# Optimization experiments

Hardware: AMD Instinct MI355X
Metric: run time of the kernel (lower is better)

Reference implementation:

```python
import jax, jax.numpy as jnp
import numpy as np

NUM_HEADS = 16
HEAD_DIM = 64  # hidden_dim // num_heads = 1024 // 16

def setup_inputs() -> dict:
    key = jax.random.key(0)
    ks = jax.random.split(key, 6)
    B, T, H, W, D = 2, 16, 24, 24, 1024
    s = 0.02
    return {
        "x": jax.random.normal(ks[0], (B, T * H * W, D), jnp.float32),
        "ws_qkv": jax.random.normal(ks[1], (D, 3 * D), jnp.float32) * s,
        "bs_qkv": jnp.zeros((3 * D,), jnp.float32),
        "ws_proj": jax.random.normal(ks[2], (D, D), jnp.float32) * s,
        "bs_proj": jnp.zeros((D,), jnp.float32),
        "wt_qkv": jax.random.normal(ks[3], (D, 3 * D), jnp.float32) * s,
        "bt_qkv": jnp.zeros((3 * D,), jnp.float32),
        "wt_proj": jax.random.normal(ks[4], (D, D), jnp.float32) * s,
        "bt_proj": jnp.zeros((D,), jnp.float32),
        "T": 16, "H": 24, "W": 24,
    }

def _heads(x):
    # [..., N, D] -> [..., nh, N, hd]
    *lead, N, D = x.shape
    x = x.reshape(*lead, N, NUM_HEADS, HEAD_DIM)
    return jnp.swapaxes(x, -2, -3)

def _attend(q, k, v, causal):
    # q,k,v: [..., nh, N, hd]
    scores = jnp.einsum("...qd,...kd->...qk", q, k) / jnp.sqrt(jnp.float32(HEAD_DIM))
    if causal:
        N = q.shape[-2]
        mask = jnp.triu(jnp.ones((N, N), bool), k=1)
        scores = jnp.where(mask, jnp.float32(-jnp.inf), scores)
    attn = jax.nn.softmax(scores, axis=-1)
    out = jnp.einsum("...qk,...kd->...qd", attn, v)
    # [..., nh, N, hd] -> [..., N, D]
    out = jnp.swapaxes(out, -2, -3)
    return out.reshape(*out.shape[:-2], NUM_HEADS * HEAD_DIM)

def _spatial(x, w_qkv, b_qkv, w_proj, b_proj, T, HW):
    B, THW, D = x.shape
    qkv = x @ w_qkv + b_qkv
    q, k, v = jnp.split(qkv, 3, axis=-1)
    # group tokens by frame: [B, T, HW, D]
    q, k, v = (t.reshape(B, T, HW, D) for t in (q, k, v))
    out = _attend(_heads(q), _heads(k), _heads(v), causal=False)
    out = out.reshape(B, THW, D)
    return out @ w_proj + b_proj

def _temporal(x, w_qkv, b_qkv, w_proj, b_proj, T, HW, causal):
    B, THW, D = x.shape
    qkv = x @ w_qkv + b_qkv
    q, k, v = jnp.split(qkv, 3, axis=-1)
    # group tokens by spatial position: [B, HW, T, D]
    q, k, v = (jnp.swapaxes(t.reshape(B, T, HW, D), 1, 2) for t in (q, k, v))
    out = _attend(_heads(q), _heads(k), _heads(v), causal=causal)  # [B, HW, T, D]
    out = jnp.swapaxes(out, 1, 2).reshape(B, THW, D)
    return out @ w_proj + b_proj

def reference(x, ws_qkv, bs_qkv, ws_proj, bs_proj, wt_qkv, bt_qkv, wt_proj, bt_proj, T, H, W):
    HW = H * W
    x = x + _spatial(x, ws_qkv, bs_qkv, ws_proj, bs_proj, T, HW)
    x = x + _temporal(x, wt_qkv, bt_qkv, wt_proj, bt_proj, T, HW, causal=True)
    return x
```

## Files before the change

kernel.cpp:

```cpp
#include <hip/hip_runtime.h>
#include <math.h>

typedef __bf16 bf16_t;
typedef unsigned char u8;
typedef __bf16 bf16x4 __attribute__((ext_vector_type(4)));
typedef __bf16 bf16x8 __attribute__((ext_vector_type(8)));
typedef float f32x4 __attribute__((ext_vector_type(4)));

#define GLDS(gp, lp) __builtin_amdgcn_global_load_lds( \
    (const __attribute__((address_space(1))) void*)(gp), \
    (__attribute__((address_space(3))) void*)(lp), 16, 0, 0)

static constexpr int B_    = 2;
static constexpr int T_    = 16;
static constexpr int HW_   = 576;
static constexpr int NH_   = 16;
static constexpr int TOK_  = B_ * T_ * HW_;
static constexpr int D_    = 1024;
static constexpr int D3_   = 3072;

#define GEMM_PROLOG_AND_KLOOP(AS, BS)                                         \
    const int tid  = threadIdx.x;                                             \
    const int lane = tid & 63, wid = tid >> 6;                                \
    const int wr   = wid >> 1, wc = wid & 1;                                  \
    const int l15  = lane & 15, lhi = lane >> 4;                              \
    const int cpx = gridDim.x >> 3;                                           \
    const int swz = (blockIdx.x & 7) * cpx + (blockIdx.x >> 3);               \
    const long row0 = (long)(swz / ntx) * 128;                                \
    const long col0 = (long)(swz % ntx) * 128;                                \
    const int  sr   = tid >> 2;                                               \
    const int  sc   = (((tid & 3) ^ ((sr >> 1) & 3)) * 8);                    \
    const bf16_t* Ag = A  + (row0 + sr) * (long)K + sc;                       \
    const bf16_t* Bg = BT + (col0 + sr) * (long)K + sc;                       \
    f32x4 acc[4][4] = {};                                                     \
    GLDS(Ag,                AS(0) + tid * 8);                                 \
    GLDS(Ag + 64 * (long)K, AS(0) + 2048 + tid * 8);                          \
    GLDS(Bg,                BS(0) + tid * 8);                                 \
    GLDS(Bg + 64 * (long)K, BS(0) + 2048 + tid * 8);                          \
    __syncthreads();                                                          \
    const int nt = K >> 5;                                                    \
    int cur = 0;                                                              \
    for (int t = 0; t < nt; ++t) {                                            \
        if (t + 1 < nt) {                                                     \
            const int k0 = (t + 1) << 5;                                      \
            GLDS(Ag + k0,                AS(cur ^ 1) + tid * 8);              \
            GLDS(Ag + 64 * (long)K + k0, AS(cur ^ 1) + 2048 + tid * 8);       \
            GLDS(Bg + k0,                BS(cur ^ 1) + tid * 8);              \
            GLDS(Bg + 64 * (long)K + k0, BS(cur ^ 1) + 2048 + tid * 8);       \
        }                                                                     \
        bf16x8 a[4], b[4];                                                    \
        _Pragma("unroll")                                                     \
        for (int i = 0; i < 4; i++) {                                         \
            const int Ra = wr * 64 + i * 16 + l15;                            \
            a[i] = *(const bf16x8*)(AS(cur) + Ra * 32                         \
                                    + ((lhi ^ ((Ra >> 1) & 3)) * 8));         \
        }                                                                     \
        _Pragma("unroll")                                                     \
        for (int j = 0; j < 4; j++) {                                         \
            const int Rb = wc * 64 + j * 16 + l15;                            \
            b[j] = *(const bf16x8*)(BS(cur) + Rb * 32                         \
                                    + ((lhi ^ ((Rb >> 1) & 3)) * 8));         \
        }                                                                     \
        __builtin_amdgcn_s_setprio(1);                                        \
        _Pragma("unroll")                                                     \
        for (int i = 0; i < 4; i++)                                           \
            _Pragma("unroll")                                                 \
            for (int j = 0; j < 4; j++)                                       \
                acc[i][j] = __builtin_amdgcn_mfma_f32_16x16x32_bf16(a[i], b[j], acc[i][j], 0, 0, 0); \
        __builtin_amdgcn_s_setprio(0);                                        \
        __syncthreads();                                                      \
        cur ^= 1;                                                             \
    }

__global__ __launch_bounds__(256) void prep(const float* __restrict__ x,
                                            u8* __restrict__ x_f8,
                                            const float* __restrict__ wqs,
                                            u8* __restrict__ wTqs8,
                                            const float* __restrict__ wps,
                                            bf16_t* __restrict__ wTps,
                                            const float* __restrict__ wqt,
                                            u8* __restrict__ wTqt8,
                                            const float* __restrict__ wpt,
                                            bf16_t* __restrict__ wTpt)
{
    const int bid = blockIdx.x, tid = threadIdx.x;
    if (bid < 4096) {
        const long n = (long)TOK_ * D_;
        for (long i = ((long)bid * 256 + tid) * 8; i < n; i += 4096L * 256 * 8) {
            const float4 v0 = *(const float4*)(x + i);
            const float4 v1 = *(const float4*)(x + i + 4);
            int lo = __builtin_amdgcn_cvt_pk_fp8_f32(v0.x, v0.y, 0, false);
            lo = __builtin_amdgcn_cvt_pk_fp8_f32(v0.z, v0.w, lo, true);
            int hi = __builtin_amdgcn_cvt_pk_fp8_f32(v1.x, v1.y, 0, false);
            hi = __builtin_amdgcn_cvt_pk_fp8_f32(v1.z, v1.w, hi, true);
            int2 p; p.x = lo; p.y = hi;
            *(int2*)(x_f8 + i) = p;
        }
        return;
    }
    const float* in; u8* out8 = nullptr; bf16_t* outb = nullptr; int C, b2;
    if (bid < 7168)       { in = wqs; out8 = wTqs8; C = 3072; b2 = bid - 4096; }
    else if (bid < 8192)  { in = wps; outb = wTps;  C = 1024; b2 = bid - 7168; }
    else if (bid < 11264) { in = wqt; out8 = wTqt8; C = 3072; b2 = bid - 8192; }
    else                  { in = wpt; outb = wTpt;  C = 1024; b2 = bid - 11264; }
    const int nbx = C >> 5;
    const int cb = (b2 % nbx) * 32, rb = (b2 / nbx) * 32;
    const int tx = tid & 31, ty = tid >> 5;
    __shared__ float tile[32][33];
    #pragma unroll
    for (int i = 0; i < 32; i += 8)
        tile[ty + i][tx] = in[(long)(rb + ty + i) * C + cb + tx];
    __syncthreads();
    if (out8) {
        #pragma unroll
        for (int i = 0; i < 32; i += 8) {
            const int p = __builtin_amdgcn_cvt_pk_fp8_f32(tile[tx][ty + i], 0.f, 0, false);
            out8[(long)(cb + ty + i) * 1024 + rb + tx] = (u8)(p & 0xff);
        }
    } else {
        #pragma unroll
        for (int i = 0; i < 32; i += 8)
            outb[(long)(cb + ty + i) * 1024 + rb + tx] = (bf16_t)tile[tx][ty + i];
    }
}

__global__ __launch_bounds__(256) void b2f8(const bf16_t* __restrict__ in,
                                            u8* __restrict__ out, long n)
{
    for (long i = ((long)blockIdx.x * 256 + threadIdx.x) * 8; i < n;
         i += (long)gridDim.x * 256 * 8) {
        bf16x8 v = *(const bf16x8*)(in + i);
        int lo = __builtin_amdgcn_cvt_pk_fp8_f32((float)v[0], (float)v[1], 0, false);
        lo = __builtin_amdgcn_cvt_pk_fp8_f32((float)v[2], (float)v[3], lo, true);
        int hi = __builtin_amdgcn_cvt_pk_fp8_f32((float)v[4], (float)v[5], 0, false);
        hi = __builtin_amdgcn_cvt_pk_fp8_f32((float)v[6], (float)v[7], hi, true);
        int2 p; p.x = lo; p.y = hi;
        *(int2*)(out + i) = p;
    }
}

__global__ __launch_bounds__(256) void gemm_f8(const u8* __restrict__ A,
                                               const u8* __restrict__ BT,
                                               const float* __restrict__ bias,
                                               bf16_t* __restrict__ Cb,
                                               bf16_t* __restrict__ vout,
                                               int vmode, int ntx,
                                               int M, int N, int K, int tperm)
{
    __shared__ bf16_t SHm[16384];
    char* SH = (char*)SHm;
    const int tid  = threadIdx.x;
    const int lane = tid & 63, wid = tid >> 6;
    const int wr   = wid >> 1, wc = wid & 1;
    const int l15  = lane & 15, lhi = lane >> 4;
    const int cpx = gridDim.x >> 3;
    const int swz = (blockIdx.x & 7) * cpx + (blockIdx.x >> 3);
    const long row0 = (long)(swz / ntx) * 128;
    const long col0 = (long)(swz % ntx) * 128;
    const int crow = tid >> 2, cq = tid & 3;

#define STG8(Xp, rbase, kt, dst) do {                                         \
        _Pragma("unroll")                                                     \
        for (int i_ = 0; i_ < 2; i_++) {                                      \
            const int row_ = crow + i_ * 64;                                  \
            GLDS(Xp + (rbase + row_) * (long)K + (kt) * 64                    \
                 + ((cq ^ ((row_ >> 1) & 3)) * 16),                           \
                 (dst) + (row_ * 64 + cq * 16));                              \
        }                                                                     \
    } while (0)

    f32x4 acc[4][4] = {};

    STG8(A,  row0, 0, SH);
    STG8(BT, col0, 0, SH + 16384);
    __syncthreads();

    const int NT = K >> 6;
    int cur = 0;
    for (int t = 0; t < NT; ++t) {
        if (t + 1 < NT) {
            STG8(A,  row0, t + 1, SH + (cur ^ 1) * 8192);
            STG8(BT, col0, t + 1, SH + 16384 + (cur ^ 1) * 8192);
        }

        long av[4][2], bv[4][2];
        #pragma unroll
        for (int i = 0; i < 4; i++) {
            const int Ra = wr * 64 + i * 16 + l15;
            const int x2 = ((Ra >> 1) & 3) << 1;
            #pragma unroll
            for (int kk = 0; kk < 2; kk++)
                av[i][kk] = *(const long*)(SH + cur * 8192 + Ra * 64
                                           + (((kk * 4 + lhi) ^ x2) * 8));
        }
        #pragma unroll
        for (int j = 0; j < 4; j++) {
            const int Rb = wc * 64 + j * 16 + l15;
            const int x2 = ((Rb >> 1) & 3) << 1;
            #pragma unroll
            for (int kk = 0; kk < 2; kk++)
                bv[j][kk] = *(const long*)(SH + 16384 + cur * 8192 + Rb * 64
                                           + (((kk * 4 + lhi) ^ x2) * 8));
        }

        __builtin_amdgcn_s_setprio(1);
        #pragma unroll
        for (int i = 0; i < 4; i++)
            #pragma unroll
            for (int j = 0; j < 4; j++) {
                acc[i][j] = __builtin_amdgcn_mfma_f32_16x16x32_fp8_fp8(av[i][0], bv[j][0], acc[i][j], 0, 0, 0);
                acc[i][j] = __builtin_amdgcn_mfma_f32_16x16x32_fp8_fp8(av[i][1], bv[j][1], acc[i][j], 0, 0, 0);
            }
        __builtin_amdgcn_s_setprio(0);
        __syncthreads();
        cur ^= 1;
    }
#undef STG8

    if (!(vmode == 1 && col0 >= 2048)) {
        #pragma unroll
        for (int i = 0; i < 4; i++) {
            #pragma unroll
            for (int j = 0; j < 4; j++) {
                const long col  = col0 + wc * 64 + j * 16 + l15;
                const int  lrow0 = wr * 64 + i * 16 + lhi * 4;
                const int  lcol  = wc * 64 + j * 16 + l15;
                #pragma unroll
                for (int r = 0; r < 4; r++)
                    SHm[(lrow0 + r) * 128 + lcol] = (bf16_t)(acc[i][j][r] + bias[col]);
            }
        }
        __syncthreads();
        #pragma unroll
        for (int k2 = 0; k2 < 8; k2++) {
            const int cc   = k2 * 256 + tid;
            const int lrow = cc >> 4, lcol = (cc & 15) * 8;
            const long row = row0 + lrow;
            long srow = row;
            if (tperm) {
                const int ri  = (int)row;
                const int bb  = ri / (T_ * HW_);
                const int rem = ri - bb * (T_ * HW_);
                const int tt  = rem / HW_;
                const int hh  = rem - tt * HW_;
                srow = ((long)bb * HW_ + hh) * T_ + tt;
            }
            *(bf16x8*)(Cb + srow * (long)N + col0 + lcol) =
                *(const bf16x8*)&SHm[lrow * 128 + lcol];
        }
        return;
    }

    #pragma unroll
    for (int i = 0; i < 4; i++) {
        #pragma unroll
        for (int j = 0; j < 4; j++) {
            const long col  = col0 + wc * 64 + j * 16 + l15;
            const long rowb = row0 + wr * 64 + i * 16 + lhi * 4;
            const int hh = ((int)col - 2048) >> 6, d = ((int)col - 2048) & 63;
            const int r0i = (int)rowb;
            const int bt0 = r0i / HW_, hw0 = r0i - bt0 * HW_;
            bf16x4 pk;
            #pragma unroll
            for (int r = 0; r < 4; r++) pk[r] = (bf16_t)(acc[i][j][r] + bias[col]);
            *(bf16x4*)(vout + ((long)(bt0 * 16 + hh) * 64 + d) * HW_ + hw0) = pk;
        }
    }
}

__global__ __launch_bounds__(256) void gemm_bt_rpp(const bf16_t* __restrict__ A,
                                                   const bf16_t* __restrict__ BT,
                                                   const float* __restrict__ bias,
                                                   const float* __restrict__ resf,
                                                   bf16_t* __restrict__ Cb,
                                                   int ntx, int M, int N, int K)
{
    __shared__ bf16_t SHm[16384];
#define As_(b) (SHm + (b) * 4096)
#define Bs_(b) (SHm + 8192 + (b) * 4096)
    GEMM_PROLOG_AND_KLOOP(As_, Bs_)

    #pragma unroll
    for (int i = 0; i < 4; i++) {
        #pragma unroll
        for (int j = 0; j < 4; j++) {
            const long col  = col0 + wc * 64 + j * 16 + l15;
            const long rowb = row0 + wr * 64 + i * 16 + lhi * 4;
            const int  lrow0 = wr * 64 + i * 16 + lhi * 4;
            const int  lcol  = wc * 64 + j * 16 + l15;
            #pragma unroll
            for (int r = 0; r < 4; r++)
                SHm[(lrow0 + r) * 128 + lcol] =
                    (bf16_t)(acc[i][j][r] + bias[col] + resf[(rowb + r) * (long)N + col]);
        }
    }
    __syncthreads();
    #pragma unroll
    for (int k2 = 0; k2 < 8; k2++) {
        const int cc   = k2 * 256 + tid;
        const int lrow = cc >> 4, lcol = (cc & 15) * 8;
        *(bf16x8*)(Cb + (row0 + lrow) * (long)N + col0 + lcol) =
            *(const bf16x8*)&SHm[lrow * 128 + lcol];
    }
#undef As_
#undef Bs_
}

__global__ __launch_bounds__(256) void gemm_bt_rpo(const bf16_t* __restrict__ A,
                                                   const bf16_t* __restrict__ BT,
                                                   const float* __restrict__ bias,
                                                   const bf16_t* __restrict__ resb,
                                                   float* __restrict__ Cf,
                                                   int ntx, int M, int N, int K)
{
    __shared__ bf16_t SHm[16384];
#define As_(b) (SHm + (b) * 4096)
#define Bs_(b) (SHm + 8192 + (b) * 4096)
    GEMM_PROLOG_AND_KLOOP(As_, Bs_)

    float* SHf = (float*)SHm;
    #pragma unroll
    for (int half = 0; half < 2; half++) {
        if (wr == half) {
            #pragma unroll
            for (int i = 0; i < 4; i++) {
                #pragma unroll
                for (int j = 0; j < 4; j++) {
                    const long col  = col0 + wc * 64 + j * 16 + l15;
                    const long rowb = row0 + wr * 64 + i * 16 + lhi * 4;
                    const int  lrow0 = i * 16 + lhi * 4;
                    const int  lcol  = wc * 64 + j * 16 + l15;
                    #pragma unroll
                    for (int r = 0; r < 4; r++)
                        SHf[(lrow0 + r) * 128 + lcol] =
                            acc[i][j][r] + bias[col]
                            + (float)resb[(rowb + r) * (long)N + col];
                }
            }
        }
        __syncthreads();
        #pragma unroll
        for (int k2 = 0; k2 < 8; k2++) {
            const int cc   = k2 * 256 + tid;
            const int lrow = cc >> 5, lc4 = (cc & 31) * 4;
            *(float4*)(Cf + (row0 + half * 64 + lrow) * (long)N + col0 + lc4) =
                *(const float4*)&SHf[lrow * 128 + lc4];
        }
        __syncthreads();
    }
#undef As_
#undef Bs_
}

__global__ __launch_bounds__(256) void attn_spatial(const bf16_t* __restrict__ qkv,
                                                    const bf16_t* __restrict__ vt,
                                                    bf16_t* __restrict__ out)
{
    __shared__ bf16_t Ks[2][64 * 64];
    __shared__ bf16_t Vts[2][64 * 64];
    __shared__ bf16_t Pws[4][16 * 72];
    const int tid = threadIdx.x, lane = tid & 63, w = tid >> 6;
    const int qt = blockIdx.x;
    const int g  = blockIdx.y;
    const int h  = g & 15, bt = g >> 4;
    const long base = (long)bt * HW_;
    const int l15 = lane & 15, lhi = lane >> 4;
    const int row0 = qt * 192 + w * 16;

    bf16x8 q[3][2];
    #pragma unroll
    for (int rg = 0; rg < 3; rg++) {
        #pragma unroll
        for (int kk = 0; kk < 2; kk++) {
            bf16x8 tq = *(const bf16x8*)(qkv + (base + row0 + rg * 64 + l15) * D3_
                                         + h * 64 + kk * 32 + lhi * 8);
            #pragma unroll
            for (int e = 0; e < 8; e++) tq[e] = (bf16_t)((float)tq[e] * 0.125f);
            q[rg][kk] = tq;
        }
    }

    const bf16_t* Kg = qkv + base * D3_ + 1024 + h * 64;
    const bf16_t* Vg = vt + (long)g * (64 * 576);

#define STAGEKV(kt, bq) do {                                                  \
        _Pragma("unroll")                                                     \
        for (int i_ = 0; i_ < 2; i_++) {                                      \
            const int c_ = i_ * 256 + tid;                                    \
            const int r_ = c_ >> 3, cb_ = (c_ & 7) << 4;                      \
            const int cs_ = cb_ ^ ((r_ & 7) << 4);                            \
            GLDS(Kg + (long)((kt) * 64 + r_) * D3_ + (cs_ >> 1),              \
                 (char*)Ks[bq] + c_ * 16);                                    \
            GLDS(Vg + (long)r_ * 576 + (kt) * 64 + (cs_ >> 1),               \
                 (char*)Vts[bq] + c_ * 16);                                   \
        }                                                                     \
    } while (0)

    float lp[3][4] = {};
    f32x4 o[3][4] = {};

    STAGEKV(0, 0);

    for (int kt = 0; kt < 9; kt++) {
        const int cur = kt & 1;
        __syncthreads();
        if (kt < 8) STAGEKV(kt + 1, cur ^ 1);

        f32x4 acc[3][4] = {};
        #pragma unroll
        for (int j = 0; j < 4; j++) {
            const int key = j * 16 + l15;
            #pragma unroll
            for (int kk = 0; kk < 2; kk++) {
                const int boff = key * 128 + ((kk * 64 + lhi * 16) ^ ((key & 7) << 4));
                bf16x8 kb = *(const bf16x8*)((const char*)Ks[cur] + boff);
                #pragma unroll
                for (int rg = 0; rg < 3; rg++)
                    acc[rg][j] = __builtin_amdgcn_mfma_f32_16x16x32_bf16(q[rg][kk], kb, acc[rg][j], 0, 0, 0);
            }
        }

        #pragma unroll
        for (int rg = 0; rg < 3; rg++) {
            #pragma unroll
            for (int r = 0; r < 4; r++) {
                const float p0 = __expf(acc[rg][0][r]);
                const float p1 = __expf(acc[rg][1][r]);
                const float p2 = __expf(acc[rg][2][r]);
                const float p3 = __expf(acc[rg][3][r]);
                lp[rg][r] += (p0 + p1) + (p2 + p3);
                const int prow = (lhi * 4 + r) * 72 + l15;
                Pws[w][prow]      = (bf16_t)p0;
                Pws[w][prow + 16] = (bf16_t)p1;
                Pws[w][prow + 32] = (bf16_t)p2;
                Pws[w][prow + 48] = (bf16_t)p3;
            }
            __builtin_amdgcn_sched_barrier(0);

            bf16x8 pa[2];
            #pragma unroll
            for (int kk = 0; kk < 2; kk++)
                pa[kk] = *(const bf16x8*)&Pws[w][l15 * 72 + kk * 32 + lhi * 8];
            #pragma unroll
            for (int j = 0; j < 4; j++) {
                const int vrow = j * 16 + l15;
                #pragma unroll
                for (int kk = 0; kk < 2; kk++) {
                    const int boff = vrow * 128 + ((kk * 64 + lhi * 16) ^ ((vrow & 7) << 4));
                    bf16x8 vb = *(const bf16x8*)((const char*)Vts[cur] + boff);
                    o[rg][j] = __builtin_amdgcn_mfma_f32_16x16x32_bf16(pa[kk], vb, o[rg][j], 0, 0, 0);
                }
            }
            __builtin_amdgcn_sched_barrier(0);
        }
    }
#undef STAGEKV

    #pragma unroll
    for (int rg = 0; rg < 3; rg++) {
        #pragma unroll
        for (int r = 0; r < 4; r++) {
            float l = lp[rg][r];
            #pragma unroll
            for (int off = 1; off < 16; off <<= 1) l += __shfl_xor(l, off);
            const float inv = 1.f / l;
            const long row = base + row0 + rg * 64 + lhi * 4 + r;
            #pragma unroll
            for (int j = 0; j < 4; j++)
                out[row * (long)D_ + h * 64 + j * 16 + l15] = (bf16_t)(o[rg][j][r] * inv);
        }
    }
}

__global__ __launch_bounds__(256) void attn_temporal(const bf16_t* __restrict__ qkv_t,
                                                     bf16_t* __restrict__ out)
{
    __shared__ bf16_t tile[16 * 1026];
    __shared__ bf16_t Plds[4][16 * 24];
    const int tid = threadIdx.x, lane = tid & 63, w = tid >> 6;
    const int l15 = lane & 15, lhi = lane >> 4;
    const int bhw = blockIdx.x;
    const int b = bhw / HW_, hw = bhw % HW_;
    const long base_row = (long)bhw * T_;
    const bf16_t* qrow = qkv_t + (base_row + l15) * D3_;

    #pragma unroll
    for (int it = 0; it < 8; it++) {
        const int c = it * 256 + tid;
        const int row = c >> 7, col = (c & 127) * 8;
        *(bf16x8*)&tile[row * 1026 + col] =
            *(const bf16x8*)(qkv_t + (base_row + row) * D3_ + 2048 + col);
    }
    __syncthreads();
    bf16x8 tv0[4], tv1[4];
    #pragma unroll
    for (int it = 0; it < 4; it++) {
        const int hd = it * 256 + tid;
        #pragma unroll
        for (int t = 0; t < 8; t++) tv0[it][t] = tile[t * 1026 + hd];
        #pragma unroll
        for (int t = 0; t < 8; t++) tv1[it][t] = tile[(8 + t) * 1026 + hd];
    }
    __syncthreads();
    #pragma unroll
    for (int it = 0; it < 4; it++) {
        const int hd = it * 256 + tid;
        *(bf16x8*)&tile[hd * 16]     = tv0[it];
        *(bf16x8*)&tile[hd * 16 + 8] = tv1[it];
    }
    __syncthreads();

    #pragma unroll
    for (int i = 0; i < 4; i++) {
        const int h = w * 4 + i;
        bf16x8 q0 = *(const bf16x8*)(qrow + h * 64 + lhi * 8);
        bf16x8 q1 = *(const bf16x8*)(qrow + h * 64 + 32 + lhi * 8);
        bf16x8 k0 = *(const bf16x8*)(qrow + 1024 + h * 64 + lhi * 8);
        bf16x8 k1 = *(const bf16x8*)(qrow + 1024 + h * 64 + 32 + lhi * 8);
        f32x4 acc = {};
        acc = __builtin_amdgcn_mfma_f32_16x16x32_bf16(q0, k0, acc, 0, 0, 0);
        acc = __builtin_amdgcn_mfma_f32_16x16x32_bf16(q1, k1, acc, 0, 0, 0);

        #pragma unroll
        for (int r = 0; r < 4; r++) {
            const int tq = lhi * 4 + r;
            float p = (l15 <= tq) ? __expf(acc[r] * 0.125f) : 0.f;
            float sum = p;
            #pragma unroll
            for (int off = 1; off < 16; off <<= 1) sum += __shfl_xor(sum, off);
            Plds[w][tq * 24 + l15] = (bf16_t)(p / sum);
        }
        __builtin_amdgcn_sched_barrier(0);

        bf16x8 pa = {};
        if (lhi < 2) pa = *(const bf16x8*)&Plds[w][l15 * 24 + lhi * 8];

        #pragma unroll
        for (int j = 0; j < 4; j++) {
            bf16x8 vb = {};
            if (lhi < 2)
                vb = *(const bf16x8*)&tile[h * 1024 + (j * 16 + l15) * 16 + lhi * 8];
            f32x4 o = {};
            o = __builtin_amdgcn_mfma_f32_16x16x32_bf16(pa, vb, o, 0, 0, 0);
            #pragma unroll
            for (int r = 0; r < 4; r++) {
                const int tq = lhi * 4 + r;
                out[(((long)b * T_ + tq) * HW_ + hw) * D_ + h * 64 + j * 16 + l15] = (bf16_t)o[r];
            }
        }
        __builtin_amdgcn_sched_barrier(0);
    }
}

extern "C" void kernel_launch(void* const* d_in, const int* in_sizes, int n_in,
                              void* d_out, int out_size, void* d_ws, size_t ws_size,
                              hipStream_t stream)
{
    const float* x       = (const float*)d_in[0];
    const float* ws_qkv  = (const float*)d_in[1];
    const float* bs_qkv  = (const float*)d_in[2];
    const float* ws_proj = (const float*)d_in[3];
    const float* bs_proj = (const float*)d_in[4];
    const float* wt_qkv  = (const float*)d_in[5];
    const float* bt_qkv  = (const float*)d_in[6];
    const float* wt_proj = (const float*)d_in[7];
    const float* bt_proj = (const float*)d_in[8];
    float* out = (float*)d_out;
    (void)in_sizes; (void)n_in; (void)out_size;

    char* ws = (char*)d_ws;
    bf16_t* qkv   = (bf16_t*)(ws);
    u8*     x_f8  = (u8*)(ws + 113246208L);
    bf16_t* att   = (bf16_t*)(ws + 113246208L);
    u8*     x1_f8 = (u8*)(ws + 113246208L);
    bf16_t* x1_bf = (bf16_t*)(ws + 150994944L);
    bf16_t* vt    = x1_bf;
    u8*     wTqs8 = (u8*)(ws + 188743680L);
    bf16_t* wTps  = (bf16_t*)(ws + 195035136L);
    u8*     wTqt8 = (u8*)(ws + 197132288L);
    bf16_t* wTpt  = (bf16_t*)(ws + 203423744L);
    if (ws_size < 205520896UL) return;

    prep<<<12288, 256, 0, stream>>>(x, x_f8, ws_qkv, wTqs8, ws_proj, wTps,
                                    wt_qkv, wTqt8, wt_proj, wTpt);

    gemm_f8<<<24 * 144, 256, 0, stream>>>(x_f8, wTqs8, bs_qkv,
                                          qkv, vt, 1, 24,
                                          TOK_, D3_, D_, 0);
    attn_spatial<<<dim3(3, 512), 256, 0, stream>>>(qkv, vt, att);
    gemm_bt_rpp<<<8 * 144, 256, 0, stream>>>(att, wTps, bs_proj, x,
                                             x1_bf, 8, TOK_, D_, D_);
    b2f8<<<4096, 256, 0, stream>>>(x1_bf, x1_f8, (long)TOK_ * D_);
    gemm_f8<<<24 * 144, 256, 0, stream>>>(x1_f8, wTqt8, bt_qkv,
                                          qkv, nullptr, 0, 24,
                                          TOK_, D3_, D_, 1);
    attn_temporal<<<1152, 256, 0, stream>>>(qkv, att);
    gemm_bt_rpo<<<8 * 144, 256, 0, stream>>>(att, wTpt, bt_proj, x1_bf,
                                             out, 8, TOK_, D_, D_);
}
```

Before: 478.0 us.

## Permute FP8 K layout so each MFMA operand pair loads as one 16-byte LDS read

The FP8 conversion kernels now write activations and QKV weights with a permuted K ordering inside each 64-element group. This lets the FP8 GEMM fetch both k-halves for an MFMA lane with a single 128-bit LDS load instead of two 64-bit loads. The LDS staging swizzle is rewritten to match, using an XOR over 16-byte slots across row pairs. The permutation must stay consistent between every producer and the consumer GEMM, and the LDS bank-conflict pattern changes.

```diff
diff --git a/kernel.cpp b/kernel.cpp
--- a/kernel.cpp
+++ b/kernel.cpp
@@ -6,6 +6,7 @@
 typedef __bf16 bf16x4 __attribute__((ext_vector_type(4)));
 typedef __bf16 bf16x8 __attribute__((ext_vector_type(8)));
 typedef float f32x4 __attribute__((ext_vector_type(4)));
+typedef long longx2 __attribute__((ext_vector_type(2)));
 
 #define GLDS(gp, lp) __builtin_amdgcn_global_load_lds( \
     (const __attribute__((address_space(1))) void*)(gp), \
@@ -18,6 +19,10 @@
 static constexpr int TOK_  = B_ * T_ * HW_;
 static constexpr int D_    = 1024;
 static constexpr int D3_   = 3072;
+
+__device__ __forceinline__ int kremap(int k) {
+    return (k & ~63) | (((k >> 3) & 3) << 4) | (((k >> 5) & 1) << 3) | (k & 7);
+}
 
 #define GEMM_PROLOG_AND_KLOOP(AS, BS)                                         \
     const int tid  = threadIdx.x;                                             \
@@ -94,7 +99,10 @@
             int hi = __builtin_amdgcn_cvt_pk_fp8_f32(v1.x, v1.y, 0, false);
             hi = __builtin_amdgcn_cvt_pk_fp8_f32(v1.z, v1.w, hi, true);
             int2 p; p.x = lo; p.y = hi;
-            *(int2*)(x_f8 + i) = p;
+            const long rb = i & ~1023L;
+            const int  g  = (int)(i & 1023) >> 3;
+            const int  pos = (g >> 3) * 64 + (g & 3) * 16 + ((g >> 2) & 1) * 8;
+            *(int2*)(x_f8 + rb + pos) = p;
         }
         return;
     }
@@ -112,10 +120,11 @@
         tile[ty + i][tx] = in[(long)(rb + ty + i) * C + cb + tx];
     __syncthreads();
     if (out8) {
+        const int kk = kremap(rb + tx);
         #pragma unroll
         for (int i = 0; i < 32; i += 8) {
             const int p = __builtin_amdgcn_cvt_pk_fp8_f32(tile[tx][ty + i], 0.f, 0, false);
-            out8[(long)(cb + ty + i) * 1024 + rb + tx] = (u8)(p & 0xff);
+            out8[(long)(cb + ty + i) * 1024 + kk] = (u8)(p & 0xff);
         }
     } else {
         #pragma unroll
@@ -135,7 +144,10 @@
         int hi = __builtin_amdgcn_cvt_pk_fp8_f32((float)v[4], (float)v[5], 0, false);
         hi = __builtin_amdgcn_cvt_pk_fp8_f32((float)v[6], (float)v[7], hi, true);
         int2 p; p.x = lo; p.y = hi;
-        *(int2*)(out + i) = p;
+        const long rb = i & ~1023L;
+        const int  g  = (int)(i & 1023) >> 3;
+        const int  pos = (g >> 3) * 64 + (g & 3) * 16 + ((g >> 2) & 1) * 8;
+        *(int2*)(out + rb + pos) = p;
     }
 }
 
@@ -157,15 +169,16 @@
     const int swz = (blockIdx.x & 7) * cpx + (blockIdx.x >> 3);
     const long row0 = (long)(swz / ntx) * 128;
     const long col0 = (long)(swz % ntx) * 128;
-    const int crow = tid >> 2, cq = tid & 3;
 
 #define STG8(Xp, rbase, kt, dst) do {                                         \
         _Pragma("unroll")                                                     \
         for (int i_ = 0; i_ < 2; i_++) {                                      \
-            const int row_ = crow + i_ * 64;                                  \
-            GLDS(Xp + (rbase + row_) * (long)K + (kt) * 64                    \
-                 + ((cq ^ ((row_ >> 1) & 3)) * 16),                           \
-                 (dst) + (row_ * 64 + cq * 16));                              \
+            const int c2_ = tid + i_ * 256;                       \
+            const int p_ = c2_ >> 3, s_ = c2_ & 7;                            \
+            const int sp_ = s_ ^ (p_ & 7);                                    \
+            const int row_ = 2 * p_ + (sp_ >> 2), q_ = sp_ & 3;               \
+            GLDS(Xp + (rbase + row_) * (long)K + (kt) * 64 + q_ * 16,         \
+                 (dst) + c2_ * 16);                                           \
         }                                                                     \
     } while (0)
 
@@ -187,20 +200,18 @@
         #pragma unroll
         for (int i = 0; i < 4; i++) {
             const int Ra = wr * 64 + i * 16 + l15;
-            const int x2 = ((Ra >> 1) & 3) << 1;
-            #pragma unroll
-            for (int kk = 0; kk < 2; kk++)
-                av[i][kk] = *(const long*)(SH + cur * 8192 + Ra * 64
-                                           + (((kk * 4 + lhi) ^ x2) * 8));
+            const int pa_ = Ra >> 1;
+            const int sa_ = (((Ra & 1) << 2) | lhi) ^ (pa_ & 7);
+            longx2 v = *(const longx2*)(SH + cur * 8192 + pa_ * 128 + sa_ * 16);
+            av[i][0] = v[0]; av[i][1] = v[1];
         }
         #pragma unroll
         for (int j = 0; j < 4; j++) {
             const int Rb = wc * 64 + j * 16 + l15;
-            const int x2 = ((Rb >> 1) & 3) << 1;
-            #pragma unroll
-            for (int kk = 0; kk < 2; kk++)
-                bv[j][kk] = *(const long*)(SH + 16384 + cur * 8192 + Rb * 64
-                                           + (((kk * 4 + lhi) ^ x2) * 8));
+            const int pb_ = Rb >> 1;
+            const int sb_ = (((Rb & 1) << 2) | lhi) ^ (pb_ & 7);
+            longx2 v = *(const longx2*)(SH + 16384 + cur * 8192 + pb_ * 128 + sb_ * 16);
+            bv[j][0] = v[0]; bv[j][1] = v[1];
         }
 
         __builtin_amdgcn_s_setprio(1);
```

Result: faster. 461.7 us (-3.4%).
